# Optimization experiments

Measured on AMD Instinct MI355X. Metric: run time of the kernel, lower is better.

## Reference

```python
import jax, jax.numpy as jnp
import numpy as np

EPS = 1e-6  # clamp epsilon in GeM
NORM_EPS = 1e-12  # torch F.normalize eps
PATCH_SIZES = (3,)


def l2norm(x, axis):
    n = jnp.sqrt(jnp.sum(x * x, axis=axis, keepdims=True))
    return x / jnp.maximum(n, NORM_EPS)


def setup_inputs() -> dict:
    key = jax.random.key(0)
    k1, k2, k3 = jax.random.split(key, 3)
    N, D, H, W, F = 16, 2048, 32, 32, 512
    x = jax.random.normal(k1, (N, D, H, W), jnp.float32)
    proj_w = jax.random.normal(k2, (F, D), jnp.float32) * (1.0 / np.sqrt(D))
    proj_b = jax.random.normal(k3, (F,), jnp.float32) * 0.01
    p = jnp.full((1,), 3.0, jnp.float32)
    return {"x": x, "proj_w": proj_w, "proj_b": proj_b, "p": p}


def reference(x, proj_w, proj_b, p):
    # ---- GeM global descriptor (global_pool path inside local_pool) ----
    x = l2norm(x, axis=1)                                  # L2 over channel dim
    g = jnp.clip(x, EPS, None) ** p[0]                     # [N,D,H,W]
    g = g.mean(axis=(-2, -1))                              # [N,D]
    g = g ** (1.0 / p[0])
    g = g @ proj_w.T + proj_b                              # [N,F]
    g = l2norm(g, axis=1)

    # ---- integral image over spatial dims ----
    integ = jnp.cumsum(jnp.cumsum(x, axis=-1), axis=-2)    # [N,D,H,W]

    local_descs = []
    for ps in PATCH_SIZES:
        off = ps // 2
        # zero-pad (1+off) on top/left, then replicate-pad off on bottom/right
        ipad = jnp.pad(integ, ((0, 0), (0, 0), (1 + off, 0), (1 + off, 0)))
        ipad = jnp.pad(ipad, ((0, 0), (0, 0), (0, off), (0, off)), mode='edge')
        # box sum via 4-corner integral-image difference
        # == grouped 2x2 conv with dilation=ps, weights [[1,-1],[-1,1]], stride=1
        box = (ipad[:, :, :-ps, :-ps] - ipad[:, :, :-ps, ps:]
               - ipad[:, :, ps:, :-ps] + ipad[:, :, ps:, ps:])  # [N,D,H,W]
        N, D, Hh, Ww = box.shape
        pd = box.reshape(N, D, Hh * Ww).transpose(0, 2, 1)  # [N,HW,D]
        pd = pd @ proj_w.T + proj_b                         # [N,HW,F]
        pd = l2norm(pd, axis=2)
        local_descs.append(pd.transpose(0, 2, 1))           # [N,F,HW]

    return g, local_descs[0]
```

## Files before the change

kernel.cpp:

```cpp
#include <hip/hip_runtime.h>
#include <hip/hip_bf16.h>

#define N_ 16
#define D_ 2048
#define H_ 32
#define W_ 32
#define HW_ 1024
#define F_ 512

typedef unsigned short u16;
typedef unsigned int u32;
typedef __attribute__((ext_vector_type(8))) short bf16x8;
typedef __attribute__((ext_vector_type(4))) float f32x4;

__device__ __forceinline__ u16 f2bf(float f) {
  union { float fv; u32 u; } c; c.fv = f;
  u32 u = c.u;
  u32 r = (u + 0x7fffu + ((u >> 16) & 1u)) >> 16;
  return (u16)r;
}

#define GLD_LDS16(gp, lp) __builtin_amdgcn_global_load_lds( \
    (const __attribute__((address_space(1))) void*)(gp), \
    (__attribute__((address_space(3))) void*)(lp), 16, 0, 0)

__global__ __launch_bounds__(256) void k_sumsq(const float* __restrict__ x, float* __restrict__ sumsq) {
  const int n = blockIdx.x;
  const int dc = blockIdx.y;
  const int t = threadIdx.x;
  const float* xp = x + ((size_t)n * D_ + (size_t)dc * 64) * HW_;
  float s0 = 0.f, s1 = 0.f, s2 = 0.f, s3 = 0.f;
  for (int d = 0; d < 64; ++d) {
    const float* row = xp + (size_t)d * HW_;
    float v0 = row[t], v1 = row[t + 256], v2 = row[t + 512], v3 = row[t + 768];
    s0 += v0 * v0; s1 += v1 * v1; s2 += v2 * v2; s3 += v3 * v3;
  }
  atomicAdd(&sumsq[n * HW_ + t      ], s0);
  atomicAdd(&sumsq[n * HW_ + t + 256], s1);
  atomicAdd(&sumsq[n * HW_ + t + 512], s2);
  atomicAdd(&sumsq[n * HW_ + t + 768], s3);
}

__global__ __launch_bounds__(256) void k_box2(const float* __restrict__ x,
    const float* __restrict__ sumsq, const float* __restrict__ pvec,
    float* __restrict__ gbuf, u16* __restrict__ boxT) {
  const int n = blockIdx.x, ht = blockIdx.y, dc = blockIdx.z;
  const int h0 = ht * 4, d0 = dc * 64;
  const int t = threadIdx.x;
  const int w = t & 31, g = t >> 5;
  const float p = pvec[0];
  const bool p3 = (p == 3.0f);

  __shared__ __align__(16) u16 sbox[128 * 68];

  float rn[6];
  #pragma unroll
  for (int jj = 0; jj < 6; ++jj) {
    int hp = h0 - 1 + jj;
    float r = 0.f;
    if (hp >= 0 && hp < H_) r = 1.0f / fmaxf(sqrtf(sumsq[n * HW_ + hp * W_ + w]), 1e-12f);
    rn[jj] = r;
  }

  float s[8];
  #pragma unroll
  for (int j = 0; j < 8; ++j) s[j] = 0.f;

  #pragma unroll 2
  for (int j = 0; j < 8; ++j) {
    const int d = d0 + g * 8 + j;
    const float* col = x + ((size_t)(n * D_ + d)) * HW_ + w;
    float v[6];
    #pragma unroll
    for (int jj = 0; jj < 6; ++jj) {
      int hp = h0 - 1 + jj;
      float xv = (hp >= 0 && hp < H_) ? col[hp * W_] : 0.f;
      v[jj] = xv * rn[jj];
    }
    #pragma unroll
    for (int jj = 1; jj <= 4; ++jj) {
      float cv = fmaxf(v[jj], 1e-6f);
      s[j] += p3 ? cv * cv * cv : __powf(cv, p);
    }
    float hs[6];
    #pragma unroll
    for (int jj = 0; jj < 6; ++jj) {
      float l = __shfl_up(v[jj], 1, 32);
      float r = __shfl_down(v[jj], 1, 32);
      if (w == 0) l = 0.f;
      if (w == 31) r = 0.f;
      hs[jj] = l + v[jj] + r;
    }
    #pragma unroll
    for (int k = 0; k < 4; ++k) {
      float b = hs[k] + hs[k + 1] + hs[k + 2];
      sbox[(k * 32 + w) * 68 + g * 8 + j] = f2bf(b);
    }
  }
  __syncthreads();

  {
    const int r = t >> 1, half = t & 1;
    const u16* srcp = sbox + r * 68 + half * 32;
    uint2 a[8];
    #pragma unroll
    for (int q = 0; q < 8; ++q) a[q] = *(const uint2*)(srcp + q * 4);
    u16* dst = boxT + ((size_t)(n * HW_ + h0 * W_ + r)) * D_ + d0 + half * 32;
    #pragma unroll
    for (int q = 0; q < 4; ++q) {
      uint4 b;
      b.x = a[2 * q].x; b.y = a[2 * q].y; b.z = a[2 * q + 1].x; b.w = a[2 * q + 1].y;
      ((uint4*)dst)[q] = b;
    }
  }

  #pragma unroll
  for (int j = 0; j < 8; ++j) {
    float v = s[j];
    v += __shfl_xor(v, 16, 32);
    v += __shfl_xor(v, 8, 32);
    v += __shfl_xor(v, 4, 32);
    v += __shfl_xor(v, 2, 32);
    v += __shfl_xor(v, 1, 32);
    if (w == 0) atomicAdd(&gbuf[n * D_ + d0 + g * 8 + j], v);
  }
}

__global__ __launch_bounds__(256) void k_wconv(const float* __restrict__ w, u16* __restrict__ wb) {
  int i = blockIdx.x * 256 + threadIdx.x;
  float4 v = ((const float4*)w)[i];
  u16 r[4] = { f2bf(v.x), f2bf(v.y), f2bf(v.z), f2bf(v.w) };
  *(uint2*)(wb + (size_t)i * 4) = *(const uint2*)r;
}

__global__ __launch_bounds__(512) void k_gemm(const u16* __restrict__ boxT,
    const u16* __restrict__ wb, const float* __restrict__ bias,
    float* __restrict__ outL) {
  const int n  = blockIdx.x >> 4;
  const int mt = blockIdx.x & 15;
  const int m0 = n * HW_ + mt * 64;
  const int hw0 = mt * 64;
  const int t = threadIdx.x;
  const int lane = t & 63, wv = t >> 6;

  __shared__ __align__(16) u16 smem[4 * 18432];
  __shared__ float s_sq[8][64];
  __shared__ float s_rn[64];

  f32x4 acc[4][4];
  #pragma unroll
  for (int a = 0; a < 4; ++a)
    #pragma unroll
    for (int b = 0; b < 4; ++b) acc[a][b] = (f32x4){0.f, 0.f, 0.f, 0.f};

  const int kswz = ((lane & 3) ^ ((lane >> 3) & 3)) * 8;
  const u16* bsrc = wb + (size_t)(wv * 64 + (lane >> 2)) * D_ + kswz;
  const u16* asrc = boxT + (size_t)(m0 + (wv & 3) * 16 + (lane >> 2)) * D_ + kswz;

  const int r15 = lane & 15;
  const int slot = ((lane >> 4) ^ ((r15 >> 1) & 3)) * 8;

#define STAGE_TILE(KT) do {                                            \
    const int k0_ = (KT) * 32;                                         \
    char* sAb_ = (char*)(smem + ((KT) & 3) * 18432);                   \
    char* sBb_ = sAb_ + 4096;                                          \
    _Pragma("unroll")                                                  \
    for (int q = 0; q < 4; ++q)                                        \
      GLD_LDS16(bsrc + (size_t)q * 16 * D_ + k0_, sBb_ + (wv * 4 + q) * 1024); \
    GLD_LDS16(asrc + k0_, sAb_ + (wv & 3) * 1024);                     \
  } while (0)

  STAGE_TILE(0);
  STAGE_TILE(1);

  for (int kt = 0; kt < 64; ++kt) {
    if (kt + 2 < 64) STAGE_TILE(kt + 2);
    __builtin_amdgcn_sched_barrier(0);
    if (kt < 62) {
      asm volatile("s_waitcnt vmcnt(10)" ::: "memory");
    } else if (kt == 62) {
      asm volatile("s_waitcnt vmcnt(5)" ::: "memory");
    } else {
      asm volatile("s_waitcnt vmcnt(0)" ::: "memory");
    }
    __builtin_amdgcn_sched_barrier(0);
    __builtin_amdgcn_s_barrier();
    __builtin_amdgcn_sched_barrier(0);

    const u16* sA = smem + (kt & 3) * 18432;
    const u16* sB = sA + 2048;
    bf16x8 af[4], bfv[4];
    #pragma unroll
    for (int mf = 0; mf < 4; ++mf)
      af[mf] = *(const bf16x8*)(sA + (mf * 16 + r15) * 32 + slot);
    #pragma unroll
    for (int nf = 0; nf < 4; ++nf)
      bfv[nf] = *(const bf16x8*)(sB + (wv * 64 + nf * 16 + r15) * 32 + slot);
    #pragma unroll
    for (int mf = 0; mf < 4; ++mf)
      #pragma unroll
      for (int nf = 0; nf < 4; ++nf)
        acc[mf][nf] = __builtin_amdgcn_mfma_f32_16x16x32_bf16(af[mf], bfv[nf], acc[mf][nf], 0, 0, 0);
  }
#undef STAGE_TILE

  float badd[4];
  #pragma unroll
  for (int nf = 0; nf < 4; ++nf) badd[nf] = bias[wv * 64 + nf * 16 + r15];
  #pragma unroll
  for (int mf = 0; mf < 4; ++mf)
    #pragma unroll
    for (int nf = 0; nf < 4; ++nf)
      #pragma unroll
      for (int j = 0; j < 4; ++j) acc[mf][nf][j] += badd[nf];

  #pragma unroll
  for (int mf = 0; mf < 4; ++mf)
    #pragma unroll
    for (int j = 0; j < 4; ++j) {
      float s = 0.f;
      #pragma unroll
      for (int nf = 0; nf < 4; ++nf) { float v = acc[mf][nf][j]; s += v * v; }
      s += __shfl_xor(s, 1); s += __shfl_xor(s, 2); s += __shfl_xor(s, 4); s += __shfl_xor(s, 8);
      if ((lane & 15) == 0) s_sq[wv][mf * 16 + (lane >> 4) * 4 + j] = s;
    }
  __syncthreads();
  if (t < 64) {
    float s = 0.f;
    #pragma unroll
    for (int w8 = 0; w8 < 8; ++w8) s += s_sq[w8][t];
    s_rn[t] = 1.0f / fmaxf(sqrtf(s), 1e-12f);
  }
  __syncthreads();

  float* ct = (float*)smem;
  for (int nf = 0; nf < 4; ++nf) {
    const int fi = wv * 16 + r15;
    #pragma unroll
    for (int mf = 0; mf < 4; ++mf)
      #pragma unroll
      for (int j = 0; j < 4; ++j) {
        int m = mf * 16 + (lane >> 4) * 4 + j;
        ct[fi * 68 + m] = acc[mf][nf][j] * s_rn[m];
      }
    __syncthreads();
    {
      int fr = t >> 2, mq = t & 3;
      int f = (fr >> 4) * 64 + nf * 16 + (fr & 15);
      float* dst = outL + ((size_t)(n * F_ + f)) * HW_ + hw0 + mq * 16;
      const float* srcp = ct + fr * 68 + mq * 16;
      float4 a0 = *(const float4*)(srcp);
      float4 a1 = *(const float4*)(srcp + 4);
      float4 a2 = *(const float4*)(srcp + 8);
      float4 a3 = *(const float4*)(srcp + 12);
      *(float4*)(dst) = a0; *(float4*)(dst + 4) = a1;
      *(float4*)(dst + 8) = a2; *(float4*)(dst + 12) = a3;
    }
    __syncthreads();
  }
}

__global__ __launch_bounds__(256) void k_gem_fin(const float* __restrict__ gbuf,
    const float* __restrict__ pvec, float* __restrict__ gg) {
  int i = blockIdx.x * 256 + threadIdx.x;
  float p = pvec[0];
  float m = gbuf[i] * (1.0f / 1024.0f);
  gg[i] = (p == 3.0f) ? cbrtf(m) : powf(m, 1.0f / p);
}

__global__ __launch_bounds__(256) void k_gproj(const float* __restrict__ w,
    const float* __restrict__ bias, const float* __restrict__ gg,
    float* __restrict__ gproj) {
  const int f = blockIdx.x;
  const int t = threadIdx.x;
  float wreg[8];
  #pragma unroll
  for (int j = 0; j < 8; ++j) wreg[j] = w[(size_t)f * D_ + t + j * 256];
  __shared__ float red[4];
  const int lane = t & 63, wv = t >> 6;
  for (int n = 0; n < N_; ++n) {
    float s = 0.f;
    #pragma unroll
    for (int j = 0; j < 8; ++j) s += wreg[j] * gg[n * D_ + t + j * 256];
    #pragma unroll
    for (int off = 32; off >= 1; off >>= 1) s += __shfl_down(s, off);
    if (lane == 0) red[wv] = s;
    __syncthreads();
    if (t == 0) gproj[n * F_ + f] = red[0] + red[1] + red[2] + red[3] + bias[f];
    __syncthreads();
  }
}

__global__ __launch_bounds__(512) void k_gnorm(const float* __restrict__ gproj, float* __restrict__ outg) {
  const int n = blockIdx.x;
  const int t = threadIdx.x;
  float v = gproj[n * F_ + t];
  float s = v * v;
  const int lane = t & 63, wv = t >> 6;
  #pragma unroll
  for (int off = 32; off >= 1; off >>= 1) s += __shfl_down(s, off);
  __shared__ float red[8];
  __shared__ float rtot;
  if (lane == 0) red[wv] = s;
  __syncthreads();
  if (t == 0) {
    float a = 0.f;
    #pragma unroll
    for (int i = 0; i < 8; ++i) a += red[i];
    rtot = 1.0f / fmaxf(sqrtf(a), 1e-12f);
  }
  __syncthreads();
  outg[n * F_ + t] = v * rtot;
}

extern "C" void kernel_launch(void* const* d_in, const int* in_sizes, int n_in,
                              void* d_out, int out_size, void* d_ws, size_t ws_size,
                              hipStream_t stream) {
  const float* x  = (const float*)d_in[0];
  const float* pw = (const float*)d_in[1];
  const float* pb = (const float*)d_in[2];
  const float* pv = (const float*)d_in[3];
  float* out = (float*)d_out;

  char* ws = (char*)d_ws;
  float* sumsq = (float*)ws;
  float* gbuf  = (float*)(ws + 65536);
  float* gg    = (float*)(ws + 65536 + 131072);
  float* gproj = (float*)(ws + 65536 + 2 * 131072);
  u16*   wb    = (u16*)(ws + 65536 + 2 * 131072 + 32768);
  u16*   boxT  = (u16*)(ws + 4u * 1024u * 1024u);

  hipMemsetAsync(d_ws, 0, 65536 + 131072, stream);

  k_sumsq<<<dim3(16, 32), dim3(256), 0, stream>>>(x, sumsq);
  k_wconv<<<dim3(1024), dim3(256), 0, stream>>>(pw, wb);
  k_box2<<<dim3(16, 8, 32), dim3(256), 0, stream>>>(x, sumsq, pv, gbuf, boxT);
  k_gem_fin<<<dim3(128), dim3(256), 0, stream>>>(gbuf, pv, gg);
  k_gproj<<<dim3(512), dim3(256), 0, stream>>>(pw, pb, gg, gproj);
  k_gnorm<<<dim3(16), dim3(512), 0, stream>>>(gproj, out);
  k_gemm<<<dim3(256), dim3(512), 0, stream>>>(boxT, wb, pb, out + N_ * F_);
}
```

Baseline: 168.6 us.

## Vectorize box-filter kernel, load GEMM weights directly to registers, replace memset

The box/GeM kernel now processes 8 rows per block, with each thread loading float4 spans along W. Horizontal neighbours are exchanged through 8-lane shuffles, which cuts halo reloads and lets each thread issue wider global loads. The GEMM stops staging weight tiles in LDS and instead prefetches B fragments from global memory straight into registers one k-step ahead, which shrinks LDS use and the async copy count. The workspace memset is replaced by a small zeroing kernel. The trade-offs are higher register pressure and B fragments served from uncoalesced global/L2 reads instead of shared memory.

```diff
diff --git a/kernel.cpp b/kernel.cpp
--- a/kernel.cpp
+++ b/kernel.cpp
@@ -24,6 +24,11 @@
     (const __attribute__((address_space(1))) void*)(gp), \
     (__attribute__((address_space(3))) void*)(lp), 16, 0, 0)
 
+__global__ __launch_bounds__(256) void k_zero(float* __restrict__ p) {
+  int i = blockIdx.x * 256 + threadIdx.x;
+  ((float4*)p)[i] = (float4){0.f, 0.f, 0.f, 0.f};
+}
+
 __global__ __launch_bounds__(256) void k_sumsq(const float* __restrict__ x, float* __restrict__ sumsq) {
   const int n = blockIdx.x;
   const int dc = blockIdx.y;
@@ -41,88 +46,110 @@
   atomicAdd(&sumsq[n * HW_ + t + 768], s3);
 }
 
-__global__ __launch_bounds__(256) void k_box2(const float* __restrict__ x,
+__global__ __launch_bounds__(256) void k_box3(const float* __restrict__ x,
     const float* __restrict__ sumsq, const float* __restrict__ pvec,
     float* __restrict__ gbuf, u16* __restrict__ boxT) {
-  const int n = blockIdx.x, ht = blockIdx.y, dc = blockIdx.z;
-  const int h0 = ht * 4, d0 = dc * 64;
-  const int t = threadIdx.x;
-  const int w = t & 31, g = t >> 5;
+  const int n = blockIdx.x, hb = blockIdx.y, dc = blockIdx.z;
+  const int h0 = hb * 8, d0 = dc * 64;
+  const int t = threadIdx.x;
+  const int w4 = t & 7, wq = w4 * 4, dg = t >> 3;
   const float p = pvec[0];
   const bool p3 = (p == 3.0f);
 
-  __shared__ __align__(16) u16 sbox[128 * 68];
-
-  float rn[6];
-  #pragma unroll
-  for (int jj = 0; jj < 6; ++jj) {
+  __shared__ __align__(16) u32 sbox[256 * 34];
+
+  float4 rn[10];
+  #pragma unroll
+  for (int jj = 0; jj < 10; ++jj) {
     int hp = h0 - 1 + jj;
-    float r = 0.f;
-    if (hp >= 0 && hp < H_) r = 1.0f / fmaxf(sqrtf(sumsq[n * HW_ + hp * W_ + w]), 1e-12f);
-    rn[jj] = r;
-  }
-
-  float s[8];
-  #pragma unroll
-  for (int j = 0; j < 8; ++j) s[j] = 0.f;
-
-  #pragma unroll 2
-  for (int j = 0; j < 8; ++j) {
-    const int d = d0 + g * 8 + j;
-    const float* col = x + ((size_t)(n * D_ + d)) * HW_ + w;
-    float v[6];
-    #pragma unroll
-    for (int jj = 0; jj < 6; ++jj) {
+    if (hp >= 0 && hp < H_) {
+      float4 ss = *(const float4*)(sumsq + n * HW_ + hp * W_ + wq);
+      rn[jj].x = 1.0f / fmaxf(sqrtf(ss.x), 1e-12f);
+      rn[jj].y = 1.0f / fmaxf(sqrtf(ss.y), 1e-12f);
+      rn[jj].z = 1.0f / fmaxf(sqrtf(ss.z), 1e-12f);
+      rn[jj].w = 1.0f / fmaxf(sqrtf(ss.w), 1e-12f);
+    } else {
+      rn[jj] = (float4){0.f, 0.f, 0.f, 0.f};
+    }
+  }
+
+  float gp[2] = {0.f, 0.f};
+  #pragma unroll
+  for (int dj = 0; dj < 2; ++dj) {
+    const int d = d0 + dg * 2 + dj;
+    const float* base = x + ((size_t)(n * D_ + d)) * HW_ + wq;
+    float4 v[10];
+    #pragma unroll
+    for (int jj = 0; jj < 10; ++jj) {
       int hp = h0 - 1 + jj;
-      float xv = (hp >= 0 && hp < H_) ? col[hp * W_] : 0.f;
-      v[jj] = xv * rn[jj];
-    }
-    #pragma unroll
-    for (int jj = 1; jj <= 4; ++jj) {
-      float cv = fmaxf(v[jj], 1e-6f);
-      s[j] += p3 ? cv * cv * cv : __powf(cv, p);
-    }
-    float hs[6];
-    #pragma unroll
-    for (int jj = 0; jj < 6; ++jj) {
-      float l = __shfl_up(v[jj], 1, 32);
-      float r = __shfl_down(v[jj], 1, 32);
-      if (w == 0) l = 0.f;
-      if (w == 31) r = 0.f;
-      hs[jj] = l + v[jj] + r;
-    }
-    #pragma unroll
-    for (int k = 0; k < 4; ++k) {
-      float b = hs[k] + hs[k + 1] + hs[k + 2];
-      sbox[(k * 32 + w) * 68 + g * 8 + j] = f2bf(b);
+      if (hp >= 0 && hp < H_) {
+        float4 xv = *(const float4*)(base + hp * W_);
+        v[jj].x = xv.x * rn[jj].x;
+        v[jj].y = xv.y * rn[jj].y;
+        v[jj].z = xv.z * rn[jj].z;
+        v[jj].w = xv.w * rn[jj].w;
+      } else {
+        v[jj] = (float4){0.f, 0.f, 0.f, 0.f};
+      }
+    }
+    float g = 0.f;
+    #pragma unroll
+    for (int jj = 1; jj <= 8; ++jj) {
+      float cx = fmaxf(v[jj].x, 1e-6f), cy = fmaxf(v[jj].y, 1e-6f);
+      float cz = fmaxf(v[jj].z, 1e-6f), cw = fmaxf(v[jj].w, 1e-6f);
+      if (p3) g += cx * cx * cx + cy * cy * cy + cz * cz * cz + cw * cw * cw;
+      else    g += __powf(cx, p) + __powf(cy, p) + __powf(cz, p) + __powf(cw, p);
+    }
+    gp[dj] = g;
+    #pragma unroll
+    for (int jj = 0; jj < 10; ++jj) {
+      float lf = __shfl_up(v[jj].w, 1, 8);
+      float rf = __shfl_down(v[jj].x, 1, 8);
+      if (w4 == 0) lf = 0.f;
+      if (w4 == 7) rf = 0.f;
+      float4 h;
+      h.x = lf + v[jj].x + v[jj].y;
+      h.y = v[jj].x + v[jj].y + v[jj].z;
+      h.z = v[jj].y + v[jj].z + v[jj].w;
+      h.w = v[jj].z + v[jj].w + rf;
+      v[jj] = h;
+    }
+    u16* sb16 = (u16*)sbox;
+    #pragma unroll
+    for (int k = 0; k < 8; ++k) {
+      float4 b;
+      b.x = v[k].x + v[k + 1].x + v[k + 2].x;
+      b.y = v[k].y + v[k + 1].y + v[k + 2].y;
+      b.z = v[k].z + v[k + 1].z + v[k + 2].z;
+      b.w = v[k].w + v[k + 1].w + v[k + 2].w;
+      const int rb = k * 32 + wq;
+      sb16[(rb + 0) * 68 + dg * 2 + dj] = f2bf(b.x);
+      sb16[(rb + 1) * 68 + dg * 2 + dj] = f2bf(b.y);
+      sb16[(rb + 2) * 68 + dg * 2 + dj] = f2bf(b.z);
+      sb16[(rb + 3) * 68 + dg * 2 + dj] = f2bf(b.w);
     }
   }
   __syncthreads();
 
   {
-    const int r = t >> 1, half = t & 1;
-    const u16* srcp = sbox + r * 68 + half * 32;
-    uint2 a[8];
-    #pragma unroll
-    for (int q = 0; q < 8; ++q) a[q] = *(const uint2*)(srcp + q * 4);
-    u16* dst = boxT + ((size_t)(n * HW_ + h0 * W_ + r)) * D_ + d0 + half * 32;
-    #pragma unroll
-    for (int q = 0; q < 4; ++q) {
-      uint4 b;
-      b.x = a[2 * q].x; b.y = a[2 * q].y; b.z = a[2 * q + 1].x; b.w = a[2 * q + 1].y;
-      ((uint4*)dst)[q] = b;
-    }
-  }
-
-  #pragma unroll
-  for (int j = 0; j < 8; ++j) {
-    float v = s[j];
-    v += __shfl_xor(v, 16, 32);
-    v += __shfl_xor(v, 8, 32);
-    v += __shfl_xor(v, 4, 32);
-    v += __shfl_xor(v, 2, 32);
-    v += __shfl_xor(v, 1, 32);
-    if (w == 0) atomicAdd(&gbuf[n * D_ + d0 + g * 8 + j], v);
+    const u32* src = sbox + t * 34;
+    u16* dst = boxT + ((size_t)(n * HW_ + h0 * W_ + t)) * D_ + d0;
+    #pragma unroll
+    for (int q = 0; q < 8; ++q) {
+      uint4 o;
+      o.x = src[q * 4 + 0]; o.y = src[q * 4 + 1];
+      o.z = src[q * 4 + 2]; o.w = src[q * 4 + 3];
+      ((uint4*)dst)[q] = o;
+    }
+  }
+
+  #pragma unroll
+  for (int dj = 0; dj < 2; ++dj) {
+    float v = gp[dj];
+    v += __shfl_xor(v, 1, 8);
+    v += __shfl_xor(v, 2, 8);
+    v += __shfl_xor(v, 4, 8);
+    if (w4 == 0) atomicAdd(&gbuf[n * D_ + d0 + dg * 2 + dj], v);
   }
 }
 
@@ -142,8 +169,9 @@
   const int hw0 = mt * 64;
   const int t = threadIdx.x;
   const int lane = t & 63, wv = t >> 6;
-
-  __shared__ __align__(16) u16 smem[4 * 18432];
+  const int r15 = lane & 15, hi = lane >> 4;
+
+  __shared__ __align__(16) float smem_f[128 * 68];
   __shared__ float s_sq[8][64];
   __shared__ float s_rn[64];
 
@@ -154,32 +182,35 @@
     for (int b = 0; b < 4; ++b) acc[a][b] = (f32x4){0.f, 0.f, 0.f, 0.f};
 
   const int kswz = ((lane & 3) ^ ((lane >> 3) & 3)) * 8;
-  const u16* bsrc = wb + (size_t)(wv * 64 + (lane >> 2)) * D_ + kswz;
   const u16* asrc = boxT + (size_t)(m0 + (wv & 3) * 16 + (lane >> 2)) * D_ + kswz;
-
-  const int r15 = lane & 15;
-  const int slot = ((lane >> 4) ^ ((r15 >> 1) & 3)) * 8;
-
-#define STAGE_TILE(KT) do {                                            \
-    const int k0_ = (KT) * 32;                                         \
-    char* sAb_ = (char*)(smem + ((KT) & 3) * 18432);                   \
-    char* sBb_ = sAb_ + 4096;                                          \
-    _Pragma("unroll")                                                  \
-    for (int q = 0; q < 4; ++q)                                        \
-      GLD_LDS16(bsrc + (size_t)q * 16 * D_ + k0_, sBb_ + (wv * 4 + q) * 1024); \
-    GLD_LDS16(asrc + k0_, sAb_ + (wv & 3) * 1024);                     \
-  } while (0)
-
-  STAGE_TILE(0);
-  STAGE_TILE(1);
+  const int slot = (hi ^ ((r15 >> 1) & 3)) * 8;
+
+  const u16* brow[4];
+  #pragma unroll
+  for (int nf = 0; nf < 4; ++nf)
+    brow[nf] = wb + (size_t)(wv * 64 + nf * 16 + r15) * D_ + hi * 8;
+
+#define STAGE_A(KT) GLD_LDS16(asrc + (size_t)(KT) * 32, \
+    (char*)smem_f + ((KT) & 3) * 4096 + (wv & 3) * 1024)
+
+  STAGE_A(0);
+  STAGE_A(1);
+  bf16x8 bc[4], bn[4];
+  #pragma unroll
+  for (int nf = 0; nf < 4; ++nf) bc[nf] = *(const bf16x8*)(brow[nf]);
 
   for (int kt = 0; kt < 64; ++kt) {
-    if (kt + 2 < 64) STAGE_TILE(kt + 2);
+    if (kt + 2 < 64) STAGE_A(kt + 2);
+    if (kt + 1 < 64) {
+      #pragma unroll
+      for (int nf = 0; nf < 4; ++nf)
+        bn[nf] = *(const bf16x8*)(brow[nf] + (kt + 1) * 32);
+    }
     __builtin_amdgcn_sched_barrier(0);
     if (kt < 62) {
-      asm volatile("s_waitcnt vmcnt(10)" ::: "memory");
+      asm volatile("s_waitcnt vmcnt(5)" ::: "memory");
     } else if (kt == 62) {
-      asm volatile("s_waitcnt vmcnt(5)" ::: "memory");
+      asm volatile("s_waitcnt vmcnt(4)" ::: "memory");
     } else {
       asm volatile("s_waitcnt vmcnt(0)" ::: "memory");
     }
@@ -187,22 +218,20 @@
     __builtin_amdgcn_s_barrier();
     __builtin_amdgcn_sched_barrier(0);
 
-    const u16* sA = smem + (kt & 3) * 18432;
-    const u16* sB = sA + 2048;
-    bf16x8 af[4], bfv[4];
+    const u16* sA = (const u16*)((const char*)smem_f + (kt & 3) * 4096);
+    bf16x8 af[4];
     #pragma unroll
     for (int mf = 0; mf < 4; ++mf)
       af[mf] = *(const bf16x8*)(sA + (mf * 16 + r15) * 32 + slot);
     #pragma unroll
-    for (int nf = 0; nf < 4; ++nf)
-      bfv[nf] = *(const bf16x8*)(sB + (wv * 64 + nf * 16 + r15) * 32 + slot);
-    #pragma unroll
     for (int mf = 0; mf < 4; ++mf)
       #pragma unroll
       for (int nf = 0; nf < 4; ++nf)
-        acc[mf][nf] = __builtin_amdgcn_mfma_f32_16x16x32_bf16(af[mf], bfv[nf], acc[mf][nf], 0, 0, 0);
-  }
-#undef STAGE_TILE
+        acc[mf][nf] = __builtin_amdgcn_mfma_f32_16x16x32_bf16(af[mf], bc[nf], acc[mf][nf], 0, 0, 0);
+    #pragma unroll
+    for (int nf = 0; nf < 4; ++nf) bc[nf] = bn[nf];
+  }
+#undef STAGE_A
 
   float badd[4];
   #pragma unroll
@@ -222,7 +251,7 @@
       #pragma unroll
       for (int nf = 0; nf < 4; ++nf) { float v = acc[mf][nf][j]; s += v * v; }
       s += __shfl_xor(s, 1); s += __shfl_xor(s, 2); s += __shfl_xor(s, 4); s += __shfl_xor(s, 8);
-      if ((lane & 15) == 0) s_sq[wv][mf * 16 + (lane >> 4) * 4 + j] = s;
+      if ((lane & 15) == 0) s_sq[wv][mf * 16 + hi * 4 + j] = s;
     }
   __syncthreads();
   if (t < 64) {
@@ -233,14 +262,14 @@
   }
   __syncthreads();
 
-  float* ct = (float*)smem;
+  float* ct = smem_f;
   for (int nf = 0; nf < 4; ++nf) {
     const int fi = wv * 16 + r15;
     #pragma unroll
     for (int mf = 0; mf < 4; ++mf)
       #pragma unroll
       for (int j = 0; j < 4; ++j) {
-        int m = mf * 16 + (lane >> 4) * 4 + j;
+        int m = mf * 16 + hi * 4 + j;
         ct[fi * 68 + m] = acc[mf][nf][j] * s_rn[m];
       }
     __syncthreads();
@@ -330,11 +359,10 @@
   u16*   wb    = (u16*)(ws + 65536 + 2 * 131072 + 32768);
   u16*   boxT  = (u16*)(ws + 4u * 1024u * 1024u);
 
-  hipMemsetAsync(d_ws, 0, 65536 + 131072, stream);
-
+  k_zero<<<dim3(48), dim3(256), 0, stream>>>(sumsq);
   k_sumsq<<<dim3(16, 32), dim3(256), 0, stream>>>(x, sumsq);
   k_wconv<<<dim3(1024), dim3(256), 0, stream>>>(pw, wb);
-  k_box2<<<dim3(16, 8, 32), dim3(256), 0, stream>>>(x, sumsq, pv, gbuf, boxT);
+  k_box3<<<dim3(16, 4, 32), dim3(256), 0, stream>>>(x, sumsq, pv, gbuf, boxT);
   k_gem_fin<<<dim3(128), dim3(256), 0, stream>>>(gbuf, pv, gg);
   k_gproj<<<dim3(512), dim3(256), 0, stream>>>(pw, pb, gg, gproj);
   k_gnorm<<<dim3(16), dim3(512), 0, stream>>>(gproj, out);
```

After: 189.3 us. 12.3% more time.

## Pre-pack GEMM operands into MFMA fragment order and load B directly to registers

Applied to the files above, without the earlier changes.

The box kernel and weight-conversion kernel now write A and B in the exact per-lane fragment order the MFMA loop consumes. The GEMM loads B fragments straight from global memory into registers with one-step register double-buffering, instead of staging B through LDS. Only A still goes through LDS, which shrinks shared memory and removes the swizzled LDS reads for B. The memset is also replaced by a small zeroing kernel. The trade-off is that every wave re-reads B from global/L2, and the wait counts must match the new load pattern.

```diff
diff --git a/kernel.cpp b/kernel.cpp
--- a/kernel.cpp
+++ b/kernel.cpp
@@ -24,6 +24,11 @@
     (const __attribute__((address_space(1))) void*)(gp), \
     (__attribute__((address_space(3))) void*)(lp), 16, 0, 0)
 
+__global__ __launch_bounds__(256) void k_zero(float* __restrict__ p) {
+  int i = blockIdx.x * 256 + threadIdx.x;
+  ((float4*)p)[i] = (float4){0.f, 0.f, 0.f, 0.f};
+}
+
 __global__ __launch_bounds__(256) void k_sumsq(const float* __restrict__ x, float* __restrict__ sumsq) {
   const int n = blockIdx.x;
   const int dc = blockIdx.y;
@@ -43,7 +48,7 @@
 
 __global__ __launch_bounds__(256) void k_box2(const float* __restrict__ x,
     const float* __restrict__ sumsq, const float* __restrict__ pvec,
-    float* __restrict__ gbuf, u16* __restrict__ boxT) {
+    float* __restrict__ gbuf, u16* __restrict__ packA) {
   const int n = blockIdx.x, ht = blockIdx.y, dc = blockIdx.z;
   const int h0 = ht * 4, d0 = dc * 64;
   const int t = threadIdx.x;
@@ -105,12 +110,15 @@
     uint2 a[8];
     #pragma unroll
     for (int q = 0; q < 8; ++q) a[q] = *(const uint2*)(srcp + q * 4);
-    u16* dst = boxT + ((size_t)(n * HW_ + h0 * W_ + r)) * D_ + d0 + half * 32;
+    const int mt = n * 16 + ht * 2 + (r >> 6);
+    const int mf = (r >> 4) & 3, r15 = r & 15;
+    const int kt = dc * 2 + half;
+    u16* dst = packA + ((size_t)(mt * 64 + kt) * 4 + mf) * 512 + r15 * 8;
     #pragma unroll
     for (int q = 0; q < 4; ++q) {
       uint4 b;
       b.x = a[2 * q].x; b.y = a[2 * q].y; b.z = a[2 * q + 1].x; b.w = a[2 * q + 1].y;
-      ((uint4*)dst)[q] = b;
+      *(uint4*)(dst + q * 128) = b;
     }
   }
 
@@ -126,24 +134,32 @@
   }
 }
 
-__global__ __launch_bounds__(256) void k_wconv(const float* __restrict__ w, u16* __restrict__ wb) {
-  int i = blockIdx.x * 256 + threadIdx.x;
-  float4 v = ((const float4*)w)[i];
-  u16 r[4] = { f2bf(v.x), f2bf(v.y), f2bf(v.z), f2bf(v.w) };
-  *(uint2*)(wb + (size_t)i * 4) = *(const uint2*)r;
-}
-
-__global__ __launch_bounds__(512) void k_gemm(const u16* __restrict__ boxT,
-    const u16* __restrict__ wb, const float* __restrict__ bias,
+__global__ __launch_bounds__(256) void k_wconv(const float* __restrict__ w, u16* __restrict__ packB) {
+  const int i = blockIdx.x * 256 + threadIdx.x;
+  const int lane = i & 63, nf = (i >> 6) & 3, kt = (i >> 8) & 63, wq = i >> 14;
+  const int r15 = lane & 15, hi = lane >> 4;
+  const int f = wq * 64 + nf * 16 + r15;
+  const int k = kt * 32 + hi * 8;
+  const float* src = w + (size_t)f * D_ + k;
+  float4 v0 = *(const float4*)(src);
+  float4 v1 = *(const float4*)(src + 4);
+  u16 r[8] = { f2bf(v0.x), f2bf(v0.y), f2bf(v0.z), f2bf(v0.w),
+               f2bf(v1.x), f2bf(v1.y), f2bf(v1.z), f2bf(v1.w) };
+  *(uint4*)(packB + (size_t)i * 8) = *(const uint4*)r;
+}
+
+__global__ __launch_bounds__(512) void k_gemm(const u16* __restrict__ packA,
+    const u16* __restrict__ packB, const float* __restrict__ bias,
     float* __restrict__ outL) {
   const int n  = blockIdx.x >> 4;
-  const int mt = blockIdx.x & 15;
-  const int m0 = n * HW_ + mt * 64;
-  const int hw0 = mt * 64;
+  const int mtl = blockIdx.x & 15;
+  const int mt = blockIdx.x;
+  const int hw0 = mtl * 64;
   const int t = threadIdx.x;
   const int lane = t & 63, wv = t >> 6;
-
-  __shared__ __align__(16) u16 smem[4 * 18432];
+  const int r15 = lane & 15, hi = lane >> 4;
+
+  __shared__ __align__(16) float smem_f[128 * 68];
   __shared__ float s_sq[8][64];
   __shared__ float s_rn[64];
 
@@ -153,33 +169,30 @@
     #pragma unroll
     for (int b = 0; b < 4; ++b) acc[a][b] = (f32x4){0.f, 0.f, 0.f, 0.f};
 
-  const int kswz = ((lane & 3) ^ ((lane >> 3) & 3)) * 8;
-  const u16* bsrc = wb + (size_t)(wv * 64 + (lane >> 2)) * D_ + kswz;
-  const u16* asrc = boxT + (size_t)(m0 + (wv & 3) * 16 + (lane >> 2)) * D_ + kswz;
-
-  const int r15 = lane & 15;
-  const int slot = ((lane >> 4) ^ ((r15 >> 1) & 3)) * 8;
-
-#define STAGE_TILE(KT) do {                                            \
-    const int k0_ = (KT) * 32;                                         \
-    char* sAb_ = (char*)(smem + ((KT) & 3) * 18432);                   \
-    char* sBb_ = sAb_ + 4096;                                          \
-    _Pragma("unroll")                                                  \
-    for (int q = 0; q < 4; ++q)                                        \
-      GLD_LDS16(bsrc + (size_t)q * 16 * D_ + k0_, sBb_ + (wv * 4 + q) * 1024); \
-    GLD_LDS16(asrc + k0_, sAb_ + (wv & 3) * 1024);                     \
-  } while (0)
-
-  STAGE_TILE(0);
-  STAGE_TILE(1);
+  const u16* asrc = packA + ((size_t)(mt * 64) * 4 + (wv & 3)) * 512 + lane * 8;
+  const u16* bbase = packB + (size_t)wv * 131072 + lane * 8;
+
+#define STAGE_A(KT) GLD_LDS16(asrc + (size_t)(KT) * 2048, \
+    (char*)smem_f + ((KT) & 3) * 4096 + (wv & 3) * 1024)
+
+  STAGE_A(0);
+  STAGE_A(1);
+  bf16x8 bc[4], bn[4];
+  #pragma unroll
+  for (int nf = 0; nf < 4; ++nf) bc[nf] = *(const bf16x8*)(bbase + nf * 512);
 
   for (int kt = 0; kt < 64; ++kt) {
-    if (kt + 2 < 64) STAGE_TILE(kt + 2);
+    if (kt + 2 < 64) STAGE_A(kt + 2);
+    if (kt + 1 < 64) {
+      #pragma unroll
+      for (int nf = 0; nf < 4; ++nf)
+        bn[nf] = *(const bf16x8*)(bbase + ((kt + 1) * 4 + nf) * 512);
+    }
     __builtin_amdgcn_sched_barrier(0);
     if (kt < 62) {
-      asm volatile("s_waitcnt vmcnt(10)" ::: "memory");
+      asm volatile("s_waitcnt vmcnt(5)" ::: "memory");
     } else if (kt == 62) {
-      asm volatile("s_waitcnt vmcnt(5)" ::: "memory");
+      asm volatile("s_waitcnt vmcnt(4)" ::: "memory");
     } else {
       asm volatile("s_waitcnt vmcnt(0)" ::: "memory");
     }
@@ -187,22 +200,20 @@
     __builtin_amdgcn_s_barrier();
     __builtin_amdgcn_sched_barrier(0);
 
-    const u16* sA = smem + (kt & 3) * 18432;
-    const u16* sB = sA + 2048;
-    bf16x8 af[4], bfv[4];
+    const u16* sA = (const u16*)((const char*)smem_f + (kt & 3) * 4096);
+    bf16x8 af[4];
     #pragma unroll
     for (int mf = 0; mf < 4; ++mf)
-      af[mf] = *(const bf16x8*)(sA + (mf * 16 + r15) * 32 + slot);
-    #pragma unroll
-    for (int nf = 0; nf < 4; ++nf)
-      bfv[nf] = *(const bf16x8*)(sB + (wv * 64 + nf * 16 + r15) * 32 + slot);
+      af[mf] = *(const bf16x8*)(sA + mf * 512 + lane * 8);
     #pragma unroll
     for (int mf = 0; mf < 4; ++mf)
       #pragma unroll
       for (int nf = 0; nf < 4; ++nf)
-        acc[mf][nf] = __builtin_amdgcn_mfma_f32_16x16x32_bf16(af[mf], bfv[nf], acc[mf][nf], 0, 0, 0);
-  }
-#undef STAGE_TILE
+        acc[mf][nf] = __builtin_amdgcn_mfma_f32_16x16x32_bf16(af[mf], bc[nf], acc[mf][nf], 0, 0, 0);
+    #pragma unroll
+    for (int nf = 0; nf < 4; ++nf) bc[nf] = bn[nf];
+  }
+#undef STAGE_A
 
   float badd[4];
   #pragma unroll
@@ -222,7 +233,7 @@
       #pragma unroll
       for (int nf = 0; nf < 4; ++nf) { float v = acc[mf][nf][j]; s += v * v; }
       s += __shfl_xor(s, 1); s += __shfl_xor(s, 2); s += __shfl_xor(s, 4); s += __shfl_xor(s, 8);
-      if ((lane & 15) == 0) s_sq[wv][mf * 16 + (lane >> 4) * 4 + j] = s;
+      if ((lane & 15) == 0) s_sq[wv][mf * 16 + hi * 4 + j] = s;
     }
   __syncthreads();
   if (t < 64) {
@@ -233,14 +244,14 @@
   }
   __syncthreads();
 
-  float* ct = (float*)smem;
+  float* ct = smem_f;
   for (int nf = 0; nf < 4; ++nf) {
     const int fi = wv * 16 + r15;
     #pragma unroll
     for (int mf = 0; mf < 4; ++mf)
       #pragma unroll
       for (int j = 0; j < 4; ++j) {
-        int m = mf * 16 + (lane >> 4) * 4 + j;
+        int m = mf * 16 + hi * 4 + j;
         ct[fi * 68 + m] = acc[mf][nf][j] * s_rn[m];
       }
     __syncthreads();
@@ -327,16 +338,15 @@
   float* gbuf  = (float*)(ws + 65536);
   float* gg    = (float*)(ws + 65536 + 131072);
   float* gproj = (float*)(ws + 65536 + 2 * 131072);
-  u16*   wb    = (u16*)(ws + 65536 + 2 * 131072 + 32768);
-  u16*   boxT  = (u16*)(ws + 4u * 1024u * 1024u);
-
-  hipMemsetAsync(d_ws, 0, 65536 + 131072, stream);
-
+  u16*   packB = (u16*)(ws + 65536 + 2 * 131072 + 32768);
+  u16*   packA = (u16*)(ws + 4u * 1024u * 1024u);
+
+  k_zero<<<dim3(48), dim3(256), 0, stream>>>(sumsq);
   k_sumsq<<<dim3(16, 32), dim3(256), 0, stream>>>(x, sumsq);
-  k_wconv<<<dim3(1024), dim3(256), 0, stream>>>(pw, wb);
-  k_box2<<<dim3(16, 8, 32), dim3(256), 0, stream>>>(x, sumsq, pv, gbuf, boxT);
+  k_wconv<<<dim3(512), dim3(256), 0, stream>>>(pw, packB);
+  k_box2<<<dim3(16, 8, 32), dim3(256), 0, stream>>>(x, sumsq, pv, gbuf, packA);
   k_gem_fin<<<dim3(128), dim3(256), 0, stream>>>(gbuf, pv, gg);
   k_gproj<<<dim3(512), dim3(256), 0, stream>>>(pw, pb, gg, gproj);
   k_gnorm<<<dim3(16), dim3(512), 0, stream>>>(gproj, out);
-  k_gemm<<<dim3(256), dim3(512), 0, stream>>>(boxT, wb, pb, out + N_ * F_);
-}
+  k_gemm<<<dim3(256), dim3(512), 0, stream>>>(packA, packB, pb, out + N_ * F_);
+}
```

Result: faster. 151.4 us (-10.2%).
